# Kernel optimization log

Hardware: AMD Instinct MI355X
Metric: run time of the kernel (lower is better)

Reference implementation:

```python
import jax, jax.numpy as jnp
import numpy as np

NUM_HEADS = 16
KERNEL_SIZE = 13  # odd, neighborhood size nh = 6


def setup_inputs() -> dict:
    key = jax.random.key(0)
    ks = jax.random.split(key, 6)
    B, L, C = 4, 4096, 512
    return {
        "x": jax.random.normal(ks[0], (B, L, C), dtype=jnp.float32),
        "qkv_w": jax.random.normal(ks[1], (3 * C, C), dtype=jnp.float32) * (C ** -0.5),
        "qkv_b": jax.random.normal(ks[2], (3 * C,), dtype=jnp.float32) * 0.02,
        "rpb": jax.random.normal(ks[3], (NUM_HEADS, 2 * KERNEL_SIZE - 1), dtype=jnp.float32) * 0.02,
        "proj_w": jax.random.normal(ks[4], (C, C), dtype=jnp.float32) * (C ** -0.5),
        "proj_b": jax.random.normal(ks[5], (C,), dtype=jnp.float32) * 0.02,
    }


def reference(x, qkv_w, qkv_b, rpb, proj_w, proj_b):
    B, L, C = x.shape
    H, K = NUM_HEADS, KERNEL_SIZE
    Dh = C // H
    scale = Dh ** -0.5
    nh = K // 2

    # qkv projection (torch Linear: x @ W.T + b)
    qkv = (x @ qkv_w.T + qkv_b).reshape(B, L, 3, H, Dh)
    qkv = jnp.transpose(qkv, (2, 0, 3, 1, 4))  # (3, B, H, L, Dh)
    q, k, v = qkv[0] * scale, qkv[1], qkv[2]

    # neighborhood indices: window of K keys, shifted (not clipped) at borders
    pos = jnp.arange(L)
    start = jnp.clip(pos - nh, 0, L - K)            # (L,)
    idx = start[:, None] + jnp.arange(K)[None, :]   # (L, K) key positions
    # relative-position-bias index: (key_pos - query_pos) + (K-1), in [0, 2K-2]
    bias_idx = idx - pos[:, None] + (K - 1)         # (L, K)

    k_g = k[:, :, idx, :]                           # (B, H, L, K, Dh)
    attn = jnp.einsum('bhld,bhlkd->bhlk', q, k_g)   # (B, H, L, K)
    attn = attn + rpb[:, bias_idx][None]            # add (H, L, K) bias
    attn = jax.nn.softmax(attn, axis=-1)

    v_g = v[:, :, idx, :]                           # (B, H, L, K, Dh)
    out = jnp.einsum('bhlk,bhlkd->bhld', attn, v_g)  # (B, H, L, Dh)
    out = jnp.transpose(out, (0, 2, 1, 3)).reshape(B, L, C)
    return out @ proj_w.T + proj_b
```

## Files before the change

kernel.cpp:

```cpp
#include <hip/hip_runtime.h>
#include <hip/hip_bf16.h>

#define BATCH   4
#define LSEQ    4096
#define CCH     512
#define HNUM    16
#define DH      32
#define KSZ     13
#define NHALF   6
#define M_TOT   16384
#define N_QKV   1536
#define KDIM    512
#define BK      64

typedef __attribute__((ext_vector_type(8))) short  short8;
typedef __attribute__((ext_vector_type(4))) short  short4_t;
typedef __attribute__((ext_vector_type(4))) float  float4_t;

__device__ __forceinline__ unsigned short f32_to_bf16(float f) {
    union { float f; unsigned int u; } un; un.f = f;
    unsigned int u = un.u;
    u += 0x7FFFu + ((u >> 16) & 1u);
    return (unsigned short)(u >> 16);
}
__device__ __forceinline__ float bf16_to_f32(unsigned short h) {
    union { unsigned int u; float f; } un; un.u = ((unsigned int)h) << 16;
    return un.f;
}

__device__ __forceinline__ void gload_lds16(const unsigned short* g, unsigned short* l) {
    __builtin_amdgcn_global_load_lds(
        (const __attribute__((address_space(1))) unsigned int*)g,
        (__attribute__((address_space(3))) unsigned int*)l,
        16, 0, 0);
}

__global__ void cvt_all(const float4_t* __restrict__ xin,  short4_t* __restrict__ xo,  int nx,
                        const float4_t* __restrict__ w1in, short4_t* __restrict__ w1o, int n1,
                        const float4_t* __restrict__ w2in, short4_t* __restrict__ w2o, int n2) {
    int i = blockIdx.x * blockDim.x + threadIdx.x;
    int stride = gridDim.x * blockDim.x;
    int ntot = nx + n1 + n2;
    for (; i < ntot; i += stride) {
        const float4_t* src; short4_t* dst; int j;
        if (i < nx)            { src = xin;  dst = xo;  j = i; }
        else if (i < nx + n1)  { src = w1in; dst = w1o; j = i - nx; }
        else                   { src = w2in; dst = w2o; j = i - nx - n1; }
        float4_t v = src[j];
        short4_t h;
        h.x = (short)f32_to_bf16(v.x);
        h.y = (short)f32_to_bf16(v.y);
        h.z = (short)f32_to_bf16(v.z);
        h.w = (short)f32_to_bf16(v.w);
        dst[j] = h;
    }
}

__global__ __launch_bounds__(256) void gemm_qkv(
    const unsigned short* __restrict__ Xb,
    const unsigned short* __restrict__ W,
    const float* __restrict__ bias,
    unsigned short* __restrict__ qkvout)
{
    extern __shared__ __align__(16) unsigned short lds[];
    const int tid  = threadIdx.x;
    const int wv   = tid >> 6, ln = tid & 63;
    const int m0   = blockIdx.x * 128;
    const int n0   = blockIdx.y * 128;
    const int wm   = (wv >> 1) * 64;
    const int wn   = (wv & 1) * 64;
    const int lr   = ln & 15;
    const int lg   = ln >> 4;
    const int rgrp = ln >> 3;
    const int csw  = ((ln & 7) ^ rgrp) * 8;

    float4_t acc[4][4];
    #pragma unroll
    for (int m = 0; m < 4; ++m)
        #pragma unroll
        for (int n = 0; n < 4; ++n)
            acc[m][n] = (float4_t){0.f, 0.f, 0.f, 0.f};

    #define STAGE(k0_, abuf_, bbuf_) do {                                     \
        _Pragma("unroll")                                                     \
        for (int it_ = 0; it_ < 4; ++it_) {                                   \
            int ch_  = it_ * 4 + wv;                 \
            int row_ = ch_ * 8 + rgrp;                                        \
            gload_lds16(Xb + (size_t)(m0 + row_) * KDIM + (k0_) + csw,        \
                        (abuf_) + ch_ * 8 * BK);                              \
            gload_lds16(W  + (size_t)(n0 + row_) * KDIM + (k0_) + csw,        \
                        (bbuf_) + ch_ * 8 * BK);                              \
        }                                                                     \
    } while (0)

    unsigned short* Ac = lds;           unsigned short* Bc = lds + 8192;
    unsigned short* An = lds + 16384;   unsigned short* Bn = lds + 24576;

    STAGE(0, Ac, Bc);

    for (int t = 0; t < 8; ++t) {
        if (t < 7) {
            STAGE((t + 1) * BK, An, Bn);
            asm volatile("s_waitcnt vmcnt(8)" ::: "memory");
        } else {
            asm volatile("s_waitcnt vmcnt(0)" ::: "memory");
        }
        __builtin_amdgcn_s_barrier();

        short8 af[2][4], bfr[2][4];
        #pragma unroll
        for (int kk = 0; kk < 2; ++kk) {
            #pragma unroll
            for (int m = 0; m < 4; ++m) {
                int row = wm + m * 16 + lr;
                int c   = (kk * 4 + lg) ^ (row & 7);
                af[kk][m] = *reinterpret_cast<const short8*>(&Ac[row * BK + c * 8]);
            }
            #pragma unroll
            for (int n = 0; n < 4; ++n) {
                int row = wn + n * 16 + lr;
                int c   = (kk * 4 + lg) ^ (row & 7);
                bfr[kk][n] = *reinterpret_cast<const short8*>(&Bc[row * BK + c * 8]);
            }
        }
        #pragma unroll
        for (int kk = 0; kk < 2; ++kk)
            #pragma unroll
            for (int m = 0; m < 4; ++m)
                #pragma unroll
                for (int n = 0; n < 4; ++n)
                    acc[m][n] = __builtin_amdgcn_mfma_f32_16x16x32_bf16(
                        af[kk][m], bfr[kk][n], acc[m][n], 0, 0, 0);

        if (t < 7) __builtin_amdgcn_s_barrier();
        unsigned short* tA = Ac; Ac = An; An = tA;
        unsigned short* tB = Bc; Bc = Bn; Bn = tB;
    }
    #undef STAGE

    const float qscale = 0.17677669529663687f;
    #pragma unroll
    for (int m = 0; m < 4; ++m) {
        #pragma unroll
        for (int n = 0; n < 4; ++n) {
            int gn    = n0 + wn + n * 16 + lr;
            int which = gn >> 9;
            int hh    = (gn >> 5) & 15;
            int dd    = gn & 31;
            float bsv = bias[gn];
            #pragma unroll
            for (int r = 0; r < 4; ++r) {
                int gm = m0 + wm + m * 16 + lg * 4 + r;
                float v = acc[m][n][r] + bsv;
                if (which == 0) v *= qscale;
                int b_ = gm >> 12, l = gm & 4095;
                size_t off = (((size_t)which * BATCH + b_) * HNUM + hh) *
                                 ((size_t)LSEQ * DH) + (size_t)l * DH + dd;
                qkvout[off] = f32_to_bf16(v);
            }
        }
    }
}

__global__ __launch_bounds__(256) void natten_fwd(
    const unsigned short* __restrict__ qkv,
    const float* __restrict__ rpb,
    unsigned short* __restrict__ ctx)
{
    __shared__ __align__(16) unsigned short ks[4 * 268 * 8];
    __shared__ __align__(16) unsigned short vs[4 * 268 * 8];
    __shared__ float rpb_s[2 * KSZ - 1];

    const int t    = threadIdx.x;
    const int lblk = blockIdx.x & 15;
    const int bh   = blockIdx.x >> 4;
    const int hh   = bh & 15, b_ = bh >> 4;
    const int l0   = lblk * 256;

    const int r0    = max(l0 - NHALF, 0);
    const int rend  = min(l0 + 256 + NHALF, LSEQ);
    const int nrows = rend - r0;

    const size_t plane = (size_t)LSEQ * DH;
    const size_t kbase = (((size_t)1 * BATCH + b_) * HNUM + hh) * plane;
    const size_t vbase = (((size_t)2 * BATCH + b_) * HNUM + hh) * plane;

    {
        const int cq  = t >> 6;
        const int rr  = t & 63;
        #pragma unroll
        for (int base = 0; base < 320; base += 64) {
            int row = base + rr;
            if (row < nrows) {
                *reinterpret_cast<short8*>(&ks[(cq * 268 + row) * 8]) =
                    *reinterpret_cast<const short8*>(&qkv[kbase + (size_t)(r0 + row) * DH + cq * 8]);
                *reinterpret_cast<short8*>(&vs[(cq * 268 + row) * 8]) =
                    *reinterpret_cast<const short8*>(&qkv[vbase + (size_t)(r0 + row) * DH + cq * 8]);
            }
        }
    }
    if (t < 2 * KSZ - 1) rpb_s[t] = rpb[hh * (2 * KSZ - 1) + t];
    __syncthreads();

    const int l = l0 + t;
    float q[DH];
    const size_t qoff = (((size_t)0 * BATCH + b_) * HNUM + hh) * plane + (size_t)l * DH;
    #pragma unroll
    for (int cq = 0; cq < 4; ++cq) {
        short8 qv = *reinterpret_cast<const short8*>(&qkv[qoff + cq * 8]);
        #pragma unroll
        for (int e = 0; e < 8; ++e) q[cq * 8 + e] = bf16_to_f32((unsigned short)qv[e]);
    }

    const int start = min(max(l - NHALF, 0), LSEQ - KSZ);
    float logit[KSZ];
    #pragma unroll
    for (int j = 0; j < KSZ; ++j) {
        int kr = start + j - r0;
        float s = 0.f;
        #pragma unroll
        for (int cq = 0; cq < 4; ++cq) {
            short8 kv = *reinterpret_cast<const short8*>(&ks[(cq * 268 + kr) * 8]);
            #pragma unroll
            for (int e = 0; e < 8; ++e)
                s += q[cq * 8 + e] * bf16_to_f32((unsigned short)kv[e]);
        }
        logit[j] = s + rpb_s[start + j - l + (KSZ - 1)];
    }
    float mx = logit[0];
    #pragma unroll
    for (int j = 1; j < KSZ; ++j) mx = fmaxf(mx, logit[j]);
    float p[KSZ], sum = 0.f;
    #pragma unroll
    for (int j = 0; j < KSZ; ++j) { p[j] = __expf(logit[j] - mx); sum += p[j]; }
    const float inv = 1.f / sum;

    float o[DH];
    #pragma unroll
    for (int d = 0; d < DH; ++d) o[d] = 0.f;
    #pragma unroll
    for (int j = 0; j < KSZ; ++j) {
        int kr = start + j - r0;
        float pj = p[j] * inv;
        #pragma unroll
        for (int cq = 0; cq < 4; ++cq) {
            short8 vv = *reinterpret_cast<const short8*>(&vs[(cq * 268 + kr) * 8]);
            #pragma unroll
            for (int e = 0; e < 8; ++e)
                o[cq * 8 + e] += pj * bf16_to_f32((unsigned short)vv[e]);
        }
    }
    const size_t obase = ((size_t)(b_ * LSEQ + l)) * CCH + hh * DH;
    #pragma unroll
    for (int cq = 0; cq < 4; ++cq) {
        short8 ov;
        #pragma unroll
        for (int e = 0; e < 8; ++e) ov[e] = (short)f32_to_bf16(o[cq * 8 + e]);
        *reinterpret_cast<short8*>(&ctx[obase + cq * 8]) = ov;
    }
}

__global__ __launch_bounds__(256) void gemm_proj(
    const unsigned short* __restrict__ Xb,
    const unsigned short* __restrict__ W,
    const float* __restrict__ bias,
    float* __restrict__ out)
{
    extern __shared__ __align__(16) unsigned short lds[];
    const int tid  = threadIdx.x;
    const int wv   = tid >> 6, ln = tid & 63;
    const int m0   = blockIdx.x * 128;
    const int n0   = blockIdx.y * 128;
    const int wm   = (wv >> 1) * 64;
    const int wn   = (wv & 1) * 64;
    const int lr   = ln & 15;
    const int lg   = ln >> 4;
    const int rgrp = ln >> 3;
    const int csw  = ((ln & 7) ^ rgrp) * 8;

    float4_t acc[4][4];
    #pragma unroll
    for (int m = 0; m < 4; ++m)
        #pragma unroll
        for (int n = 0; n < 4; ++n)
            acc[m][n] = (float4_t){0.f, 0.f, 0.f, 0.f};

    #define STAGEP(k0_, abuf_, bbuf_) do {                                    \
        _Pragma("unroll")                                                     \
        for (int it_ = 0; it_ < 4; ++it_) {                                   \
            int ch_  = it_ * 4 + wv;                                          \
            int row_ = ch_ * 8 + rgrp;                                        \
            gload_lds16(Xb + (size_t)(m0 + row_) * KDIM + (k0_) + csw,        \
                        (abuf_) + ch_ * 8 * BK);                              \
            gload_lds16(W  + (size_t)(n0 + row_) * KDIM + (k0_) + csw,        \
                        (bbuf_) + ch_ * 8 * BK);                              \
        }                                                                     \
    } while (0)

    unsigned short* Ac = lds;           unsigned short* Bc = lds + 8192;
    unsigned short* An = lds + 16384;   unsigned short* Bn = lds + 24576;

    STAGEP(0, Ac, Bc);

    for (int t = 0; t < 8; ++t) {
        if (t < 7) {
            STAGEP((t + 1) * BK, An, Bn);
            asm volatile("s_waitcnt vmcnt(8)" ::: "memory");
        } else {
            asm volatile("s_waitcnt vmcnt(0)" ::: "memory");
        }
        __builtin_amdgcn_s_barrier();

        short8 af[2][4], bfr[2][4];
        #pragma unroll
        for (int kk = 0; kk < 2; ++kk) {
            #pragma unroll
            for (int m = 0; m < 4; ++m) {
                int row = wm + m * 16 + lr;
                int c   = (kk * 4 + lg) ^ (row & 7);
                af[kk][m] = *reinterpret_cast<const short8*>(&Ac[row * BK + c * 8]);
            }
            #pragma unroll
            for (int n = 0; n < 4; ++n) {
                int row = wn + n * 16 + lr;
                int c   = (kk * 4 + lg) ^ (row & 7);
                bfr[kk][n] = *reinterpret_cast<const short8*>(&Bc[row * BK + c * 8]);
            }
        }
        #pragma unroll
        for (int kk = 0; kk < 2; ++kk)
            #pragma unroll
            for (int m = 0; m < 4; ++m)
                #pragma unroll
                for (int n = 0; n < 4; ++n)
                    acc[m][n] = __builtin_amdgcn_mfma_f32_16x16x32_bf16(
                        af[kk][m], bfr[kk][n], acc[m][n], 0, 0, 0);

        if (t < 7) __builtin_amdgcn_s_barrier();
        unsigned short* tA = Ac; Ac = An; An = tA;
        unsigned short* tB = Bc; Bc = Bn; Bn = tB;
    }
    #undef STAGEP

    #pragma unroll
    for (int m = 0; m < 4; ++m) {
        #pragma unroll
        for (int n = 0; n < 4; ++n) {
            int gn = n0 + wn + n * 16 + lr;
            float bsv = bias[gn];
            #pragma unroll
            for (int r = 0; r < 4; ++r) {
                int gm = m0 + wm + m * 16 + lg * 4 + r;
                out[(size_t)gm * CCH + gn] = acc[m][n][r] + bsv;
            }
        }
    }
}

extern "C" void kernel_launch(void* const* d_in, const int* in_sizes, int n_in,
                              void* d_out, int out_size, void* d_ws, size_t ws_size,
                              hipStream_t stream) {
    const float* x      = (const float*)d_in[0];
    const float* qkv_w  = (const float*)d_in[1];
    const float* qkv_b  = (const float*)d_in[2];
    const float* rpb    = (const float*)d_in[3];
    const float* proj_w = (const float*)d_in[4];
    const float* proj_b = (const float*)d_in[5];
    float* out = (float*)d_out;
    char* ws = (char*)d_ws;

    unsigned short* qkv = (unsigned short*)(ws);
    unsigned short* xb  = (unsigned short*)(ws + 50331648);
    unsigned short* ctx = (unsigned short*)(ws + 50331648);
    unsigned short* wq  = (unsigned short*)(ws + 67108864);
    unsigned short* wp  = (unsigned short*)(ws + 68681728);

    cvt_all<<<2048, 256, 0, stream>>>(
        (const float4_t*)x,      (short4_t*)xb, M_TOT * KDIM / 4,
        (const float4_t*)qkv_w,  (short4_t*)wq, 786432 / 4,
        (const float4_t*)proj_w, (short4_t*)wp, 262144 / 4);

    dim3 g1(M_TOT / 128, N_QKV / 128);
    gemm_qkv<<<g1, 256, 65536, stream>>>(xb, wq, qkv_b, qkv);

    natten_fwd<<<BATCH * HNUM * (LSEQ / 256), 256, 0, stream>>>(qkv, rpb, ctx);

    dim3 g2(M_TOT / 128, CCH / 128);
    gemm_proj<<<g2, 256, 65536, stream>>>(ctx, wp, proj_b, out);
}
```

Before: 79.42 us.

## Enlarge QKV GEMM tile to 256x128 with split-stage BK=32 pipelining

The QKV projection GEMM now uses 256x128 block tiles (each wave computes 128x64) with a K step of 32. Each step's global-to-LDS prefetch is split into two halves interleaved with the two MFMA sub-phases. It also adds s_setprio around the MFMA bursts and a min-2-blocks launch bound, and cuts LDS to 48KB so occupancy can rise. The goal is more operand reuse per LDS load and better overlap of memory with compute, at the cost of doubled accumulator registers and more barriers per K step.

```diff
diff --git a/kernel.cpp b/kernel.cpp
--- a/kernel.cpp
+++ b/kernel.cpp
@@ -56,7 +56,7 @@
     }
 }
 
-__global__ __launch_bounds__(256) void gemm_qkv(
+__global__ __launch_bounds__(256, 2) void gemm_qkv(
     const unsigned short* __restrict__ Xb,
     const unsigned short* __restrict__ W,
     const float* __restrict__ bias,
@@ -65,93 +65,112 @@
     extern __shared__ __align__(16) unsigned short lds[];
     const int tid  = threadIdx.x;
     const int wv   = tid >> 6, ln = tid & 63;
-    const int m0   = blockIdx.x * 128;
+    const int m0   = blockIdx.x * 256;
     const int n0   = blockIdx.y * 128;
-    const int wm   = (wv >> 1) * 64;
+    const int wm   = (wv >> 1) * 128;
     const int wn   = (wv & 1) * 64;
     const int lr   = ln & 15;
     const int lg   = ln >> 4;
-    const int rgrp = ln >> 3;
-    const int csw  = ((ln & 7) ^ rgrp) * 8;
-
-    float4_t acc[4][4];
-    #pragma unroll
-    for (int m = 0; m < 4; ++m)
+    const int r16  = ln >> 2;
+    const int csw4 = ((ln & 3) ^ (r16 & 3)) * 8;
+
+    float4_t acc[8][4];
+    #pragma unroll
+    for (int m = 0; m < 8; ++m)
         #pragma unroll
         for (int n = 0; n < 4; ++n)
             acc[m][n] = (float4_t){0.f, 0.f, 0.f, 0.f};
 
-    #define STAGE(k0_, abuf_, bbuf_) do {                                     \
+    #define STAGE_HALF(k0_, d_, h_) do {                                      \
         _Pragma("unroll")                                                     \
-        for (int it_ = 0; it_ < 4; ++it_) {                                   \
-            int ch_  = it_ * 4 + wv;                 \
-            int row_ = ch_ * 8 + rgrp;                                        \
-            gload_lds16(Xb + (size_t)(m0 + row_) * KDIM + (k0_) + csw,        \
-                        (abuf_) + ch_ * 8 * BK);                              \
-            gload_lds16(W  + (size_t)(n0 + row_) * KDIM + (k0_) + csw,        \
-                        (bbuf_) + ch_ * 8 * BK);                              \
+        for (int i_ = 0; i_ < 2; ++i_) {                                      \
+            int g_ = wv * 4 + (h_) * 2 + i_;               \
+            gload_lds16(Xb + (size_t)(m0 + g_ * 16 + r16) * KDIM + (k0_) + csw4,\
+                        lds + (d_) * 12288 + g_ * 512);                       \
+        }                                                                     \
+        {                                                                     \
+            int g_ = wv * 2 + (h_);                         \
+            gload_lds16(W + (size_t)(n0 + g_ * 16 + r16) * KDIM + (k0_) + csw4,\
+                        lds + (d_) * 12288 + 8192 + g_ * 512);                \
         }                                                                     \
     } while (0)
 
-    unsigned short* Ac = lds;           unsigned short* Bc = lds + 8192;
-    unsigned short* An = lds + 16384;   unsigned short* Bn = lds + 24576;
-
-    STAGE(0, Ac, Bc);
-
-    for (int t = 0; t < 8; ++t) {
-        if (t < 7) {
-            STAGE((t + 1) * BK, An, Bn);
-            asm volatile("s_waitcnt vmcnt(8)" ::: "memory");
+    STAGE_HALF(0, 0, 0);
+    STAGE_HALF(0, 0, 1);
+
+    #pragma unroll 2
+    for (int t = 0; t < 16; ++t) {
+        const int b = t & 1;
+        const unsigned short* Ab = lds + b * 12288;
+        const unsigned short* Bb = lds + b * 12288 + 8192;
+
+        if (t < 15) {
+            STAGE_HALF((t + 1) * 32, b ^ 1, 0);
+            asm volatile("s_waitcnt vmcnt(3)" ::: "memory");
         } else {
             asm volatile("s_waitcnt vmcnt(0)" ::: "memory");
         }
         __builtin_amdgcn_s_barrier();
 
-        short8 af[2][4], bfr[2][4];
-        #pragma unroll
-        for (int kk = 0; kk < 2; ++kk) {
-            #pragma unroll
-            for (int m = 0; m < 4; ++m) {
-                int row = wm + m * 16 + lr;
-                int c   = (kk * 4 + lg) ^ (row & 7);
-                af[kk][m] = *reinterpret_cast<const short8*>(&Ac[row * BK + c * 8]);
-            }
-            #pragma unroll
-            for (int n = 0; n < 4; ++n) {
-                int row = wn + n * 16 + lr;
-                int c   = (kk * 4 + lg) ^ (row & 7);
-                bfr[kk][n] = *reinterpret_cast<const short8*>(&Bc[row * BK + c * 8]);
-            }
-        }
-        #pragma unroll
-        for (int kk = 0; kk < 2; ++kk)
-            #pragma unroll
-            for (int m = 0; m < 4; ++m)
-                #pragma unroll
-                for (int n = 0; n < 4; ++n)
-                    acc[m][n] = __builtin_amdgcn_mfma_f32_16x16x32_bf16(
-                        af[kk][m], bfr[kk][n], acc[m][n], 0, 0, 0);
-
-        if (t < 7) __builtin_amdgcn_s_barrier();
-        unsigned short* tA = Ac; Ac = An; An = tA;
-        unsigned short* tB = Bc; Bc = Bn; Bn = tB;
-    }
-    #undef STAGE
+        short8 bfr[4], af[4];
+        #pragma unroll
+        for (int n = 0; n < 4; ++n) {
+            int row = wn + n * 16 + lr;
+            bfr[n] = *reinterpret_cast<const short8*>(
+                &Bb[row * 32 + (lg ^ (row & 3)) * 8]);
+        }
+        #pragma unroll
+        for (int m = 0; m < 4; ++m) {
+            int row = wm + m * 16 + lr;
+            af[m] = *reinterpret_cast<const short8*>(
+                &Ab[row * 32 + (lg ^ (row & 3)) * 8]);
+        }
+        __builtin_amdgcn_s_setprio(1);
+        #pragma unroll
+        for (int m = 0; m < 4; ++m)
+            #pragma unroll
+            for (int n = 0; n < 4; ++n)
+                acc[m][n] = __builtin_amdgcn_mfma_f32_16x16x32_bf16(
+                    af[m], bfr[n], acc[m][n], 0, 0, 0);
+        __builtin_amdgcn_s_setprio(0);
+        __builtin_amdgcn_sched_barrier(0);
+
+        if (t < 15) STAGE_HALF((t + 1) * 32, b ^ 1, 1);
+
+        short8 af2[4];
+        #pragma unroll
+        for (int m = 0; m < 4; ++m) {
+            int row = wm + 64 + m * 16 + lr;
+            af2[m] = *reinterpret_cast<const short8*>(
+                &Ab[row * 32 + (lg ^ (row & 3)) * 8]);
+        }
+        __builtin_amdgcn_s_setprio(1);
+        #pragma unroll
+        for (int m = 0; m < 4; ++m)
+            #pragma unroll
+            for (int n = 0; n < 4; ++n)
+                acc[4 + m][n] = __builtin_amdgcn_mfma_f32_16x16x32_bf16(
+                    af2[m], bfr[n], acc[4 + m][n], 0, 0, 0);
+        __builtin_amdgcn_s_setprio(0);
+
+        __builtin_amdgcn_s_barrier();
+    }
+    #undef STAGE_HALF
 
     const float qscale = 0.17677669529663687f;
     #pragma unroll
-    for (int m = 0; m < 4; ++m) {
-        #pragma unroll
-        for (int n = 0; n < 4; ++n) {
-            int gn    = n0 + wn + n * 16 + lr;
+    for (int mf = 0; mf < 8; ++mf) {
+        #pragma unroll
+        for (int nf = 0; nf < 4; ++nf) {
+            int gn    = n0 + wn + nf * 16 + lr;
             int which = gn >> 9;
             int hh    = (gn >> 5) & 15;
             int dd    = gn & 31;
             float bsv = bias[gn];
             #pragma unroll
             for (int r = 0; r < 4; ++r) {
-                int gm = m0 + wm + m * 16 + lg * 4 + r;
-                float v = acc[m][n][r] + bsv;
+                int gm = m0 + wm + mf * 16 + lg * 4 + r;
+                float v = acc[mf][nf][r] + bsv;
                 if (which == 0) v *= qscale;
                 int b_ = gm >> 12, l = gm & 4095;
                 size_t off = (((size_t)which * BATCH + b_) * HNUM + hh) *
@@ -380,8 +399,8 @@
         (const float4_t*)qkv_w,  (short4_t*)wq, 786432 / 4,
         (const float4_t*)proj_w, (short4_t*)wp, 262144 / 4);
 
-    dim3 g1(M_TOT / 128, N_QKV / 128);
-    gemm_qkv<<<g1, 256, 65536, stream>>>(xb, wq, qkv_b, qkv);
+    dim3 g1(M_TOT / 256, N_QKV / 128);
+    gemm_qkv<<<g1, 256, 49152, stream>>>(xb, wq, qkv_b, qkv);
 
     natten_fwd<<<BATCH * HNUM * (LSEQ / 256), 256, 0, stream>>>(qkv, rpb, ctx);
 
```

Result: slower. 83.50 us (+5.1%).

## Compute neighborhood attention with MFMA over 16-query, 32-key banded tiles

Applied to the files above, without the earlier changes.

Replaces the scalar per-thread QK dot products and PV accumulation in the neighborhood attention kernel with bf16 MFMA instructions. Each wave handles 16 queries at a time against a 32-key band, masks logits outside each query's window, and does the softmax with lane shuffles. Probabilities are staged in LDS, and V is stored transposed in LDS so it can feed the second MFMA. This trades scalar FMA work for redundant matrix work on the masked band, and adds small uncoalesced bf16 output stores and extra shuffles.

```diff
diff --git a/kernel.cpp b/kernel.cpp
--- a/kernel.cpp
+++ b/kernel.cpp
@@ -84,7 +84,7 @@
     #define STAGE(k0_, abuf_, bbuf_) do {                                     \
         _Pragma("unroll")                                                     \
         for (int it_ = 0; it_ < 4; ++it_) {                                   \
-            int ch_  = it_ * 4 + wv;                 \
+            int ch_  = it_ * 4 + wv;                                          \
             int row_ = ch_ * 8 + rgrp;                                        \
             gload_lds16(Xb + (size_t)(m0 + row_) * KDIM + (k0_) + csw,        \
                         (abuf_) + ch_ * 8 * BK);                              \
@@ -167,97 +167,103 @@
     const float* __restrict__ rpb,
     unsigned short* __restrict__ ctx)
 {
-    __shared__ __align__(16) unsigned short ks[4 * 268 * 8];
-    __shared__ __align__(16) unsigned short vs[4 * 268 * 8];
-    __shared__ float rpb_s[2 * KSZ - 1];
+    #define NRP 280
+    __shared__ __align__(16) unsigned short vt[DH * NRP];
+    __shared__ __align__(16) unsigned short pl[4 * 16 * 32];
+    __shared__ float rpb_s[25];
 
     const int t    = threadIdx.x;
+    const int wv   = t >> 6, ln = t & 63;
     const int lblk = blockIdx.x & 15;
     const int bh   = blockIdx.x >> 4;
     const int hh   = bh & 15, b_ = bh >> 4;
-    const int l0   = lblk * 256;
-
-    const int r0    = max(l0 - NHALF, 0);
-    const int rend  = min(l0 + 256 + NHALF, LSEQ);
-    const int nrows = rend - r0;
+    const int l0b  = lblk * 256;
+    const int r0   = l0b - 6;
 
     const size_t plane = (size_t)LSEQ * DH;
+    const size_t qbase = (((size_t)0 * BATCH + b_) * HNUM + hh) * plane;
     const size_t kbase = (((size_t)1 * BATCH + b_) * HNUM + hh) * plane;
     const size_t vbase = (((size_t)2 * BATCH + b_) * HNUM + hh) * plane;
 
-    {
-        const int cq  = t >> 6;
-        const int rr  = t & 63;
-        #pragma unroll
-        for (int base = 0; base < 320; base += 64) {
-            int row = base + rr;
-            if (row < nrows) {
-                *reinterpret_cast<short8*>(&ks[(cq * 268 + row) * 8]) =
-                    *reinterpret_cast<const short8*>(&qkv[kbase + (size_t)(r0 + row) * DH + cq * 8]);
-                *reinterpret_cast<short8*>(&vs[(cq * 268 + row) * 8]) =
-                    *reinterpret_cast<const short8*>(&qkv[vbase + (size_t)(r0 + row) * DH + cq * 8]);
-            }
-        }
-    }
-    if (t < 2 * KSZ - 1) rpb_s[t] = rpb[hh * (2 * KSZ - 1) + t];
+    for (int kr = t; kr < 276; kr += 256) {
+        int ka = min(max(r0 + kr, 0), LSEQ - 1);
+        #pragma unroll
+        for (int cq = 0; cq < 4; ++cq) {
+            short8 v = *reinterpret_cast<const short8*>(&qkv[vbase + (size_t)ka * DH + cq * 8]);
+            #pragma unroll
+            for (int e = 0; e < 8; ++e)
+                vt[(cq * 8 + e) * NRP + kr] = (unsigned short)v[e];
+        }
+    }
+    if (t < 25) rpb_s[t] = rpb[hh * 25 + t];
     __syncthreads();
 
-    const int l = l0 + t;
-    float q[DH];
-    const size_t qoff = (((size_t)0 * BATCH + b_) * HNUM + hh) * plane + (size_t)l * DH;
-    #pragma unroll
-    for (int cq = 0; cq < 4; ++cq) {
-        short8 qv = *reinterpret_cast<const short8*>(&qkv[qoff + cq * 8]);
-        #pragma unroll
-        for (int e = 0; e < 8; ++e) q[cq * 8 + e] = bf16_to_f32((unsigned short)qv[e]);
-    }
-
-    const int start = min(max(l - NHALF, 0), LSEQ - KSZ);
-    float logit[KSZ];
-    #pragma unroll
-    for (int j = 0; j < KSZ; ++j) {
-        int kr = start + j - r0;
-        float s = 0.f;
-        #pragma unroll
-        for (int cq = 0; cq < 4; ++cq) {
-            short8 kv = *reinterpret_cast<const short8*>(&ks[(cq * 268 + kr) * 8]);
-            #pragma unroll
-            for (int e = 0; e < 8; ++e)
-                s += q[cq * 8 + e] * bf16_to_f32((unsigned short)kv[e]);
-        }
-        logit[j] = s + rpb_s[start + j - l + (KSZ - 1)];
-    }
-    float mx = logit[0];
-    #pragma unroll
-    for (int j = 1; j < KSZ; ++j) mx = fmaxf(mx, logit[j]);
-    float p[KSZ], sum = 0.f;
-    #pragma unroll
-    for (int j = 0; j < KSZ; ++j) { p[j] = __expf(logit[j] - mx); sum += p[j]; }
-    const float inv = 1.f / sum;
-
-    float o[DH];
-    #pragma unroll
-    for (int d = 0; d < DH; ++d) o[d] = 0.f;
-    #pragma unroll
-    for (int j = 0; j < KSZ; ++j) {
-        int kr = start + j - r0;
-        float pj = p[j] * inv;
-        #pragma unroll
-        for (int cq = 0; cq < 4; ++cq) {
-            short8 vv = *reinterpret_cast<const short8*>(&vs[(cq * 268 + kr) * 8]);
-            #pragma unroll
-            for (int e = 0; e < 8; ++e)
-                o[cq * 8 + e] += pj * bf16_to_f32((unsigned short)vv[e]);
-        }
-    }
-    const size_t obase = ((size_t)(b_ * LSEQ + l)) * CCH + hh * DH;
-    #pragma unroll
-    for (int cq = 0; cq < 4; ++cq) {
-        short8 ov;
-        #pragma unroll
-        for (int e = 0; e < 8; ++e) ov[e] = (short)f32_to_bf16(o[cq * 8 + e]);
-        *reinterpret_cast<short8*>(&ctx[obase + cq * 8]) = ov;
-    }
+    const int g = ln >> 4;
+    const int c = ln & 15;
+
+    #pragma unroll
+    for (int qi = 0; qi < 4; ++qi) {
+        const int l0 = l0b + wv * 64 + qi * 16;
+        const int k0 = l0 - 6;
+
+        short8 qf = *reinterpret_cast<const short8*>(
+            &qkv[qbase + (size_t)(l0 + c) * DH + g * 8]);
+        int key0c = min(max(k0 + c, 0), LSEQ - 1);
+        int key1c = min(max(k0 + 16 + c, 0), LSEQ - 1);
+        short8 kf0 = *reinterpret_cast<const short8*>(
+            &qkv[kbase + (size_t)key0c * DH + g * 8]);
+        short8 kf1 = *reinterpret_cast<const short8*>(
+            &qkv[kbase + (size_t)key1c * DH + g * 8]);
+        float4_t s0 = (float4_t){0.f, 0.f, 0.f, 0.f};
+        float4_t s1 = (float4_t){0.f, 0.f, 0.f, 0.f};
+        s0 = __builtin_amdgcn_mfma_f32_16x16x32_bf16(qf, kf0, s0, 0, 0, 0);
+        s1 = __builtin_amdgcn_mfma_f32_16x16x32_bf16(qf, kf1, s1, 0, 0, 0);
+
+        const int ka0 = k0 + c;
+        const int ka1 = k0 + 16 + c;
+        #pragma unroll
+        for (int r = 0; r < 4; ++r) {
+            int tok = l0 + g * 4 + r;
+            int st  = min(max(tok - NHALF, 0), LSEQ - KSZ);
+            bool v0 = (ka0 >= st) && (ka0 < st + KSZ);
+            bool v1 = (ka1 >= st) && (ka1 < st + KSZ);
+            float b0 = rpb_s[min(max(ka0 - tok + 12, 0), 24)];
+            float b1 = rpb_s[min(max(ka1 - tok + 12, 0), 24)];
+            float x0 = v0 ? s0[r] + b0 : -1e30f;
+            float x1 = v1 ? s1[r] + b1 : -1e30f;
+            float m = fmaxf(x0, x1);
+            #pragma unroll
+            for (int d = 1; d < 16; d <<= 1) m = fmaxf(m, __shfl_xor(m, d));
+            float e0 = v0 ? __expf(x0 - m) : 0.f;
+            float e1 = v1 ? __expf(x1 - m) : 0.f;
+            float s = e0 + e1;
+            #pragma unroll
+            for (int d = 1; d < 16; d <<= 1) s += __shfl_xor(s, d);
+            float inv = 1.f / s;
+            pl[wv * 512 + (g * 4 + r) * 32 + c]      = f32_to_bf16(e0 * inv);
+            pl[wv * 512 + (g * 4 + r) * 32 + 16 + c] = f32_to_bf16(e1 * inv);
+        }
+
+        short8 pa = *reinterpret_cast<const short8*>(
+            &pl[wv * 512 + c * 32 + g * 8]);
+        int k0rel = l0 - l0b;
+        short8 vb0 = *reinterpret_cast<const short8*>(
+            &vt[c * NRP + k0rel + g * 8]);
+        short8 vb1 = *reinterpret_cast<const short8*>(
+            &vt[(16 + c) * NRP + k0rel + g * 8]);
+        float4_t o0 = (float4_t){0.f, 0.f, 0.f, 0.f};
+        float4_t o1 = (float4_t){0.f, 0.f, 0.f, 0.f};
+        o0 = __builtin_amdgcn_mfma_f32_16x16x32_bf16(pa, vb0, o0, 0, 0, 0);
+        o1 = __builtin_amdgcn_mfma_f32_16x16x32_bf16(pa, vb1, o1, 0, 0, 0);
+
+        #pragma unroll
+        for (int r = 0; r < 4; ++r) {
+            size_t ob = ((size_t)(b_ * LSEQ + l0 + g * 4 + r)) * CCH + hh * DH;
+            ctx[ob + c]      = f32_to_bf16(o0[r]);
+            ctx[ob + 16 + c] = f32_to_bf16(o1[r]);
+        }
+    }
+    #undef NRP
 }
 
 __global__ __launch_bounds__(256) void gemm_proj(
```

Measured after the change: 76.79 us, median of 3. -3.3%, faster.
